# Performance work log

Hardware: AMD Instinct MI355X
Metric: run time of the kernel (lower is better)

Reference implementation:

```python
import jax, jax.numpy as jnp
import numpy as np

N = 50000
E = 800000
EPS = 1e-5


def graph_conv(x, src, dst, ew, W_rel, b_rel, W_root):
    # PyG GraphConv (aggr='add'): lin_rel(sum_j e_ij * x_j) + lin_root(x_i)
    msg = x[src] * ew[:, None]                      # [E, F_in]
    agg = jax.ops.segment_sum(msg, dst, num_segments=N)  # [N, F_in]
    return agg @ W_rel.T + b_rel + x @ W_root.T


def batchnorm_relu(h, gamma, beta):
    mu = jnp.mean(h, axis=0)
    var = jnp.mean(jnp.square(h - mu), axis=0)
    hn = (h - mu) * jax.lax.rsqrt(var + EPS)
    return jax.nn.relu(hn * gamma + beta)


def setup_inputs() -> dict:
    key = jax.random.key(0)
    ks = jax.random.split(key, 16)
    d_in, h, d_out = 128, 256, 64

    def lin(k, fo, fi):
        return jax.random.normal(k, (fo, fi), jnp.float32) * (1.0 / np.sqrt(fi))

    return {
        "x": jax.random.normal(ks[0], (N, d_in), jnp.float32),
        "edge_index": jax.random.randint(ks[1], (2, E), 0, N, jnp.int32),
        "edge_weight": jax.random.uniform(ks[2], (E,), jnp.float32),
        "Wr0": lin(ks[3], h, d_in), "br0": jnp.zeros((h,), jnp.float32), "Wt0": lin(ks[4], h, d_in),
        "g0": jnp.ones((h,), jnp.float32), "be0": jnp.zeros((h,), jnp.float32),
        "Wr1": lin(ks[5], h, h), "br1": jnp.zeros((h,), jnp.float32), "Wt1": lin(ks[6], h, h),
        "g1": jnp.ones((h,), jnp.float32), "be1": jnp.zeros((h,), jnp.float32),
        "Wr2": lin(ks[7], d_out, h), "br2": jnp.zeros((d_out,), jnp.float32), "Wt2": lin(ks[8], d_out, h),
    }


def reference(x, edge_index, edge_weight, Wr0, br0, Wt0, g0, be0,
              Wr1, br1, Wt1, g1, be1, Wr2, br2, Wt2):
    src, dst = edge_index[0], edge_index[1]
    h = graph_conv(x, src, dst, edge_weight, Wr0, br0, Wt0)
    h = batchnorm_relu(h, g0, be0)
    h = graph_conv(h, src, dst, edge_weight, Wr1, br1, Wt1)
    h = batchnorm_relu(h, g1, be1)
    return graph_conv(h, src, dst, edge_weight, Wr2, br2, Wt2)
```

## Files before the change

### kernel.cpp

```cpp
#include <hip/hip_runtime.h>
#include <cstddef>
#include <cstdint>

#define SCAN_B 512

using bf16x8 = __attribute__((ext_vector_type(8))) short;
using f32x4  = __attribute__((ext_vector_type(4))) float;

__device__ __forceinline__ unsigned short f2bf(float f) {
    unsigned int u = __builtin_bit_cast(unsigned int, f);
    return (unsigned short)((u + 0x7FFFu + ((u >> 16) & 1u)) >> 16);
}
__device__ __forceinline__ float bf2f(unsigned short b) {
    unsigned int u = ((unsigned int)b) << 16;
    return __builtin_bit_cast(float, u);
}
__device__ __forceinline__ float i2f(int i) { return __builtin_bit_cast(float, i); }
__device__ __forceinline__ void gload_lds16(const void* g, void* l) {
    __builtin_amdgcn_global_load_lds((const __attribute__((address_space(1))) void*)g,
                                     (__attribute__((address_space(3))) void*)l, 16, 0, 0);
}

__global__ void hist_rank_k(const int* __restrict__ dst, int* __restrict__ counts,
                            int* __restrict__ rank, int E) {
    int e = blockIdx.x * blockDim.x + threadIdx.x;
    if (e >= E) return;
    rank[e] = atomicAdd(&counts[dst[e]], 1);
}

__global__ void scan1_k(const int* __restrict__ counts, int* __restrict__ partial,
                        int* __restrict__ blocksum, int Nn) {
    __shared__ int sh[SCAN_B];
    int i = blockIdx.x * SCAN_B + threadIdx.x;
    int v = (i < Nn) ? counts[i] : 0;
    sh[threadIdx.x] = v;
    __syncthreads();
    for (int off = 1; off < SCAN_B; off <<= 1) {
        int t = (threadIdx.x >= (unsigned)off) ? sh[threadIdx.x - off] : 0;
        __syncthreads();
        sh[threadIdx.x] += t;
        __syncthreads();
    }
    if (i < Nn) partial[i] = sh[threadIdx.x];
    if (threadIdx.x == SCAN_B - 1) blocksum[blockIdx.x] = sh[threadIdx.x];
}

__global__ void scan2_k(int* __restrict__ blocksum, int nb) {
    __shared__ int sh[256];
    int v = (threadIdx.x < (unsigned)nb) ? blocksum[threadIdx.x] : 0;
    sh[threadIdx.x] = v;
    __syncthreads();
    for (int off = 1; off < 256; off <<= 1) {
        int t = (threadIdx.x >= (unsigned)off) ? sh[threadIdx.x - off] : 0;
        __syncthreads();
        sh[threadIdx.x] += t;
        __syncthreads();
    }
    if (threadIdx.x < (unsigned)nb) blocksum[threadIdx.x] = sh[threadIdx.x];
}

__global__ void scan3_k(const int* __restrict__ partial, const int* __restrict__ blocksum,
                        int* __restrict__ offsets, int Nn) {
    int i = blockIdx.x * SCAN_B + threadIdx.x;
    if (i >= Nn) return;
    int add = (blockIdx.x > 0) ? blocksum[blockIdx.x - 1] : 0;
    offsets[i + 1] = partial[i] + add;
    if (i == 0) offsets[0] = 0;
}

__global__ void fill2_k(const int* __restrict__ src, const int* __restrict__ dst,
                        const float* __restrict__ ew, const int* __restrict__ offsets,
                        const int* __restrict__ rank, int2* __restrict__ e_sw, int E) {
    int e = blockIdx.x * blockDim.x + threadIdx.x;
    if (e >= E) return;
    int d = dst[e];
    int pos = offsets[d] + rank[e];
    e_sw[pos] = make_int2(src[e], __builtin_bit_cast(int, ew[e]));
}

__global__ void f2bf_all_k(const float* __restrict__ x, const float* __restrict__ Wr0,
                           const float* __restrict__ Wt0, const float* __restrict__ Wr1,
                           const float* __restrict__ Wt1, const float* __restrict__ Wr2,
                           const float* __restrict__ Wt2, unsigned short* __restrict__ x_bf,
                           unsigned short* __restrict__ Wr0b, unsigned short* __restrict__ Wt0b,
                           unsigned short* __restrict__ Wr1b, unsigned short* __restrict__ Wt1b,
                           unsigned short* __restrict__ Wr2b, unsigned short* __restrict__ Wt2b,
                           int n4x) {
    int j = blockIdx.x * blockDim.x + threadIdx.x;
    const float* s;
    unsigned short* d;
    if (j < n4x) { s = x; d = x_bf; }
    else {
        j -= n4x;
        if (j < 8192) { s = Wr0; d = Wr0b; }
        else { j -= 8192;
        if (j < 8192) { s = Wt0; d = Wt0b; }
        else { j -= 8192;
        if (j < 16384) { s = Wr1; d = Wr1b; }
        else { j -= 16384;
        if (j < 16384) { s = Wt1; d = Wt1b; }
        else { j -= 16384;
        if (j < 4096) { s = Wr2; d = Wr2b; }
        else { j -= 4096;
        if (j >= 4096) return;
        s = Wt2; d = Wt2b; } } } } }
    }
    float4 v = reinterpret_cast<const float4*>(s)[j];
    ushort4 o;
    o.x = f2bf(v.x); o.y = f2bf(v.y); o.z = f2bf(v.z); o.w = f2bf(v.w);
    reinterpret_cast<ushort4*>(d)[j] = o;
}

template<int F>
__global__ void gather_bf_k(const unsigned short* __restrict__ x, const int* __restrict__ offsets,
                            const int2* __restrict__ e_sw, unsigned short* __restrict__ agg, int Nn) {
    int wid = (blockIdx.x * blockDim.x + threadIdx.x) >> 6;
    int lane = threadIdx.x & 63;
    if (wid >= Nn) return;
    int p = offsets[wid], end = offsets[wid + 1];
    if constexpr (F == 256) {
        float a0 = 0.f, a1 = 0.f, a2 = 0.f, a3 = 0.f;
        for (; p + 8 <= end; p += 8) {
            int2 ee[8];
            #pragma unroll
            for (int i = 0; i < 8; ++i) ee[i] = e_sw[p + i];
            ushort4 vv[8];
            #pragma unroll
            for (int i = 0; i < 8; ++i)
                vv[i] = *reinterpret_cast<const ushort4*>(x + (size_t)ee[i].x * F + lane * 4);
            #pragma unroll
            for (int i = 0; i < 8; ++i) {
                float w = i2f(ee[i].y);
                a0 += w * bf2f(vv[i].x); a1 += w * bf2f(vv[i].y);
                a2 += w * bf2f(vv[i].z); a3 += w * bf2f(vv[i].w);
            }
        }
        for (; p + 4 <= end; p += 4) {
            int2 ee[4];
            #pragma unroll
            for (int i = 0; i < 4; ++i) ee[i] = e_sw[p + i];
            ushort4 vv[4];
            #pragma unroll
            for (int i = 0; i < 4; ++i)
                vv[i] = *reinterpret_cast<const ushort4*>(x + (size_t)ee[i].x * F + lane * 4);
            #pragma unroll
            for (int i = 0; i < 4; ++i) {
                float w = i2f(ee[i].y);
                a0 += w * bf2f(vv[i].x); a1 += w * bf2f(vv[i].y);
                a2 += w * bf2f(vv[i].z); a3 += w * bf2f(vv[i].w);
            }
        }
        for (; p < end; ++p) {
            int2 e0 = e_sw[p];
            ushort4 v0 = *reinterpret_cast<const ushort4*>(x + (size_t)e0.x * F + lane * 4);
            float w0 = i2f(e0.y);
            a0 += w0 * bf2f(v0.x); a1 += w0 * bf2f(v0.y);
            a2 += w0 * bf2f(v0.z); a3 += w0 * bf2f(v0.w);
        }
        ushort4 o;
        o.x = f2bf(a0); o.y = f2bf(a1); o.z = f2bf(a2); o.w = f2bf(a3);
        *reinterpret_cast<ushort4*>(agg + (size_t)wid * F + lane * 4) = o;
    } else {
        float a0 = 0.f, a1 = 0.f;
        for (; p + 8 <= end; p += 8) {
            int2 ee[8];
            #pragma unroll
            for (int i = 0; i < 8; ++i) ee[i] = e_sw[p + i];
            unsigned int vv[8];
            #pragma unroll
            for (int i = 0; i < 8; ++i)
                vv[i] = *reinterpret_cast<const unsigned int*>(x + (size_t)ee[i].x * F + lane * 2);
            #pragma unroll
            for (int i = 0; i < 8; ++i) {
                float w = i2f(ee[i].y);
                a0 += w * bf2f((unsigned short)vv[i]);
                a1 += w * bf2f((unsigned short)(vv[i] >> 16));
            }
        }
        for (; p < end; ++p) {
            int2 e0 = e_sw[p];
            unsigned int v0 = *reinterpret_cast<const unsigned int*>(x + (size_t)e0.x * F + lane * 2);
            float w0 = i2f(e0.y);
            a0 += w0 * bf2f((unsigned short)v0);
            a1 += w0 * bf2f((unsigned short)(v0 >> 16));
        }
        unsigned int o = (unsigned int)f2bf(a0) | ((unsigned int)f2bf(a1) << 16);
        *reinterpret_cast<unsigned int*>(agg + (size_t)wid * F + lane * 2) = o;
    }
}

__global__ void gather_out_k(const unsigned short* __restrict__ t, const float* __restrict__ root,
                             const int* __restrict__ offsets, const int2* __restrict__ e_sw,
                             float* __restrict__ out, int Nn) {
    int gt = blockIdx.x * blockDim.x + threadIdx.x;
    int node = gt >> 4;
    int li = gt & 15;
    if (node >= Nn) return;
    int p = offsets[node], end = offsets[node + 1];
    float a0 = 0.f, a1 = 0.f, a2 = 0.f, a3 = 0.f;
    for (; p + 8 <= end; p += 8) {
        int2 ee[8];
        #pragma unroll
        for (int i = 0; i < 8; ++i) ee[i] = e_sw[p + i];
        ushort4 vv[8];
        #pragma unroll
        for (int i = 0; i < 8; ++i)
            vv[i] = *reinterpret_cast<const ushort4*>(t + (size_t)ee[i].x * 64 + li * 4);
        #pragma unroll
        for (int i = 0; i < 8; ++i) {
            float w = i2f(ee[i].y);
            a0 += w * bf2f(vv[i].x); a1 += w * bf2f(vv[i].y);
            a2 += w * bf2f(vv[i].z); a3 += w * bf2f(vv[i].w);
        }
    }
    for (; p < end; ++p) {
        int2 e0 = e_sw[p];
        ushort4 v0 = *reinterpret_cast<const ushort4*>(t + (size_t)e0.x * 64 + li * 4);
        float w0 = i2f(e0.y);
        a0 += w0 * bf2f(v0.x); a1 += w0 * bf2f(v0.y);
        a2 += w0 * bf2f(v0.z); a3 += w0 * bf2f(v0.w);
    }
    float4 r = *reinterpret_cast<const float4*>(root + (size_t)node * 64 + li * 4);
    float4 o = make_float4(r.x + a0, r.y + a1, r.z + a2, r.w + a3);
    *reinterpret_cast<float4*>(out + (size_t)node * 64 + li * 4) = o;
}

template<int K, int O, int BM, int BN, int MODE>
__global__ __launch_bounds__(256) void gemm_mfma_k(
        const unsigned short* __restrict__ A, const unsigned short* __restrict__ Wa,
        const unsigned short* __restrict__ X, const unsigned short* __restrict__ Wb,
        const float* __restrict__ bias, unsigned short* __restrict__ out_bf,
        float* __restrict__ out_f, float* __restrict__ sums, float* __restrict__ sumsq,
        int Nn) {
    constexpr int MI = BM / 16;
    constexpr int OJ = BN / 64;
    constexpr int KSTEPS = K / 64;
    constexpr int NT = (MODE == 0 ? 2 : 1) * KSTEPS;
    constexpr int ACH = BM / 32;
    constexpr int BCH = BN / 32;
    __shared__ unsigned short As[2][BM * 64];
    __shared__ unsigned short Bs[2][BN * 64];
    const int tid = threadIdx.x;
    const int w = tid >> 6, l = tid & 63;
    const int lrow = l & 15, kgrp = l >> 4;
    int bx = blockIdx.x;
    bx = (bx & 7) * (gridDim.x >> 3) + (bx >> 3);
    const int m0 = bx * BM;
    const int n0 = blockIdx.y * BN;

    auto stage = [&](int buf, int t) {
        int ph = t / KSTEPS;
        int k0 = (t % KSTEPS) * 64;
        const unsigned short* Ap = (MODE == 0 && ph) ? X : A;
        const unsigned short* Wp = (MODE == 0 && ph) ? Wb : Wa;
        #pragma unroll
        for (int i = 0; i < ACH; ++i) {
            int c = i * 256 + tid;
            int row = c >> 3, slot = c & 7;
            gload_lds16(Ap + (size_t)(m0 + row) * K + k0 + ((slot ^ (row & 7)) << 3),
                        &As[buf][(i * 256 + w * 64) * 8]);
        }
        #pragma unroll
        for (int i = 0; i < BCH; ++i) {
            int c = i * 256 + tid;
            int row = c >> 3, slot = c & 7;
            gload_lds16(Wp + (size_t)(n0 + row) * K + k0 + ((slot ^ (row & 7)) << 3),
                        &Bs[buf][(i * 256 + w * 64) * 8]);
        }
    };

    f32x4 acc[MI][OJ];
    #pragma unroll
    for (int i = 0; i < MI; ++i)
        #pragma unroll
        for (int j = 0; j < OJ; ++j) {
            f32x4 z = {0.f, 0.f, 0.f, 0.f};
            acc[i][j] = z;
        }

    stage(0, 0);
    __syncthreads();
    #pragma unroll
    for (int t = 0; t < NT; ++t) {
        const int cur = t & 1;
        if (t + 1 < NT) stage(cur ^ 1, t + 1);
        #pragma unroll
        for (int ks = 0; ks < 2; ++ks) {
            bf16x8 a[MI], b[OJ];
            #pragma unroll
            for (int mi = 0; mi < MI; ++mi) {
                int row = mi * 16 + lrow;
                int slot = (ks * 4 + kgrp) ^ (row & 7);
                a[mi] = *reinterpret_cast<const bf16x8*>(&As[cur][row * 64 + slot * 8]);
            }
            #pragma unroll
            for (int oj = 0; oj < OJ; ++oj) {
                int row = w * (OJ * 16) + oj * 16 + lrow;
                int slot = (ks * 4 + kgrp) ^ (row & 7);
                b[oj] = *reinterpret_cast<const bf16x8*>(&Bs[cur][row * 64 + slot * 8]);
            }
            #pragma unroll
            for (int mi = 0; mi < MI; ++mi)
                #pragma unroll
                for (int oj = 0; oj < OJ; ++oj)
                    acc[mi][oj] = __builtin_amdgcn_mfma_f32_16x16x32_bf16(
                        a[mi], b[oj], acc[mi][oj], 0, 0, 0);
        }
        __syncthreads();
    }

    if constexpr (MODE == 0) {
        #pragma unroll
        for (int oj = 0; oj < OJ; ++oj) {
            int col = n0 + w * (OJ * 16) + oj * 16 + lrow;
            float bcol = bias[col];
            float s = 0.f, q = 0.f;
            #pragma unroll
            for (int mi = 0; mi < MI; ++mi) {
                #pragma unroll
                for (int r = 0; r < 4; ++r) {
                    int row = m0 + mi * 16 + kgrp * 4 + r;
                    float v = acc[mi][oj][r] + bcol;
                    if (row < Nn) {
                        out_bf[(size_t)row * O + col] = f2bf(v);
                        s += v; q += v * v;
                    }
                }
            }
            s += __shfl_xor(s, 16, 64); q += __shfl_xor(q, 16, 64);
            s += __shfl_xor(s, 32, 64); q += __shfl_xor(q, 32, 64);
            if (kgrp == 0) {
                atomicAdd(&sums[col], s);
                atomicAdd(&sumsq[col], q);
            }
        }
    } else {
        #pragma unroll
        for (int oj = 0; oj < OJ; ++oj) {
            int col = n0 + w * (OJ * 16) + oj * 16 + lrow;
            #pragma unroll
            for (int mi = 0; mi < MI; ++mi) {
                #pragma unroll
                for (int r = 0; r < 4; ++r) {
                    int row = m0 + mi * 16 + kgrp * 4 + r;
                    if (row < Nn) {
                        if (col < 64)
                            out_bf[(size_t)row * 64 + col] = f2bf(acc[mi][oj][r]);
                        else
                            out_f[(size_t)row * 64 + (col - 64)] = acc[mi][oj][r] + bias[col - 64];
                    }
                }
            }
        }
    }
}

__global__ void bn_coef_k(const float* __restrict__ sums, const float* __restrict__ sumsq,
                          const float* __restrict__ g, const float* __restrict__ be,
                          float* __restrict__ scale, float* __restrict__ shift, float invN) {
    int f = threadIdx.x;
    float mu = sums[f] * invN;
    float var = sumsq[f] * invN - mu * mu;
    float sc = g[f] * rsqrtf(var + 1e-5f);
    scale[f] = sc;
    shift[f] = be[f] - mu * sc;
}

__global__ void bn_relu_bf_k(const unsigned short* __restrict__ h, const float* __restrict__ scale,
                             const float* __restrict__ shift, unsigned short* __restrict__ hb,
                             int total4) {
    int t = blockIdx.x * blockDim.x + threadIdx.x;
    if (t >= total4) return;
    int f0 = (t & 63) * 4;
    ushort4 v = reinterpret_cast<const ushort4*>(h)[t];
    float4 sc = *reinterpret_cast<const float4*>(scale + f0);
    float4 sh = *reinterpret_cast<const float4*>(shift + f0);
    ushort4 o;
    o.x = f2bf(fmaxf(bf2f(v.x) * sc.x + sh.x, 0.f));
    o.y = f2bf(fmaxf(bf2f(v.y) * sc.y + sh.y, 0.f));
    o.z = f2bf(fmaxf(bf2f(v.z) * sc.z + sh.z, 0.f));
    o.w = f2bf(fmaxf(bf2f(v.w) * sc.w + sh.w, 0.f));
    reinterpret_cast<ushort4*>(hb)[t] = o;
}

extern "C" void kernel_launch(void* const* d_in, const int* in_sizes, int n_in,
                              void* d_out, int out_size, void* d_ws, size_t ws_size,
                              hipStream_t stream) {
    const float* x   = (const float*)d_in[0];
    const int*   ei  = (const int*)d_in[1];
    const float* ew  = (const float*)d_in[2];
    const float* Wr0 = (const float*)d_in[3];
    const float* br0 = (const float*)d_in[4];
    const float* Wt0 = (const float*)d_in[5];
    const float* g0  = (const float*)d_in[6];
    const float* be0 = (const float*)d_in[7];
    const float* Wr1 = (const float*)d_in[8];
    const float* br1 = (const float*)d_in[9];
    const float* Wt1 = (const float*)d_in[10];
    const float* g1  = (const float*)d_in[11];
    const float* be1 = (const float*)d_in[12];
    const float* Wr2 = (const float*)d_in[13];
    const float* br2 = (const float*)d_in[14];
    const float* Wt2 = (const float*)d_in[15];

    const int E  = in_sizes[2];
    const int Nn = in_sizes[0] / 128;
    const size_t NP = 50176;
    const int* src = ei;
    const int* dst = ei + E;

    unsigned short* x_bf   = (unsigned short*)d_ws;
    unsigned short* agg_bf = x_bf + NP * 128;
    unsigned short* h0N    = agg_bf + NP * 256;
    unsigned short* h1N    = h0N + NP * 256;
    unsigned short* h_bf   = h1N + NP * 256;
    unsigned short* t_bf   = h_bf + NP * 256;
    unsigned short* wbf    = t_bf + NP * 64;
    unsigned short* Wr0b = wbf;
    unsigned short* Wt0b = wbf + 32768;
    unsigned short* Wr1b = wbf + 65536;
    unsigned short* Wt1b = wbf + 131072;
    unsigned short* W2cat = wbf + 196608;
    float* root  = (float*)(wbf + 229376);
    int2*  e_sw  = (int2*)(root + NP * 64);
    float* stats = (float*)(e_sw + E);
    int*   counts  = (int*)(stats + 4096);
    int*   partial = counts + Nn;
    int*   blocksum = partial + Nn;
    int*   rank    = blocksum + 512;
    int*   offsets = rank + E;

    dim3 blk(256);
    const int nbScan = (Nn + SCAN_B - 1) / SCAN_B;
    const float invN = 1.0f / (float)Nn;
    const int n4x = Nn * 32;

    hipMemsetAsync(stats, 0, (4096 + (size_t)Nn) * sizeof(float), stream);

    hist_rank_k<<<dim3((E + 255) / 256), blk, 0, stream>>>(dst, counts, rank, E);
    scan1_k<<<dim3(nbScan), dim3(SCAN_B), 0, stream>>>(counts, partial, blocksum, Nn);
    scan2_k<<<dim3(1), dim3(256), 0, stream>>>(blocksum, nbScan);
    scan3_k<<<dim3(nbScan), dim3(SCAN_B), 0, stream>>>(partial, blocksum, offsets, Nn);
    fill2_k<<<dim3((E + 255) / 256), blk, 0, stream>>>(src, dst, ew, offsets, rank, e_sw, E);

    f2bf_all_k<<<dim3((n4x + 57344 + 255) / 256), blk, 0, stream>>>(
        x, Wr0, Wt0, Wr1, Wt1, Wr2, Wt2,
        x_bf, Wr0b, Wt0b, Wr1b, Wt1b, W2cat, W2cat + 16384, n4x);

    const int gatherBlocks = (Nn * 64 + 255) / 256;

    gather_bf_k<128><<<dim3(gatherBlocks), blk, 0, stream>>>(x_bf, offsets, e_sw, agg_bf, Nn);
    gemm_mfma_k<128, 256, 128, 128, 0><<<dim3(NP / 128, 2), blk, 0, stream>>>(
        agg_bf, Wr0b, x_bf, Wt0b, br0, h_bf, nullptr, stats + 0, stats + 256, Nn);
    bn_coef_k<<<dim3(1), blk, 0, stream>>>(stats + 0, stats + 256, g0, be0,
                                           stats + 512, stats + 768, invN);
    bn_relu_bf_k<<<dim3((Nn * 64 + 255) / 256), blk, 0, stream>>>(
        h_bf, stats + 512, stats + 768, h0N, Nn * 64);

    gather_bf_k<256><<<dim3(gatherBlocks), blk, 0, stream>>>(h0N, offsets, e_sw, agg_bf, Nn);
    gemm_mfma_k<256, 256, 128, 128, 0><<<dim3(NP / 128, 2), blk, 0, stream>>>(
        agg_bf, Wr1b, h0N, Wt1b, br1, h_bf, nullptr, stats + 1024, stats + 1280, Nn);
    bn_coef_k<<<dim3(1), blk, 0, stream>>>(stats + 1024, stats + 1280, g1, be1,
                                           stats + 1536, stats + 1792, invN);
    bn_relu_bf_k<<<dim3((Nn * 64 + 255) / 256), blk, 0, stream>>>(
        h_bf, stats + 1536, stats + 1792, h1N, Nn * 64);

    gemm_mfma_k<256, 128, 128, 128, 1><<<dim3(NP / 128, 1), blk, 0, stream>>>(
        h1N, W2cat, nullptr, nullptr, br2, t_bf, root, nullptr, nullptr, Nn);
    gather_out_k<<<dim3((Nn * 16 + 255) / 256), blk, 0, stream>>>(
        t_bf, root, offsets, e_sw, (float*)d_out, Nn);
}
```

Before: 313.9 us.

## Fuse histogram with conversion, fold BN coefs, widen GEMM blocks, tidy gather addressing

The edge histogram and the fp32-to-bf16 conversion now run as one kernel, and the BN coefficient kernel is folded into bn_relu, which removes several launches. The GEMM moves to 512-thread blocks with a 2x4 wave grid, so each wave holds fewer accumulator tiles. The gather kernels use 32-bit byte-offset addressing, a scalar wave id and bit-mask bf16 unpacking, and the 4-edge unrolled tail loop is dropped. The trade-offs are that per-element BN recomputes rsqrt in every thread, and the GEMM register and occupancy behaviour changes.

```diff
diff --git a/kernel.cpp b/kernel.cpp
--- a/kernel.cpp
+++ b/kernel.cpp
@@ -16,77 +16,28 @@
     return __builtin_bit_cast(float, u);
 }
 __device__ __forceinline__ float i2f(int i) { return __builtin_bit_cast(float, i); }
+__device__ __forceinline__ float u2f(unsigned int u) { return __builtin_bit_cast(float, u); }
 __device__ __forceinline__ void gload_lds16(const void* g, void* l) {
     __builtin_amdgcn_global_load_lds((const __attribute__((address_space(1))) void*)g,
                                      (__attribute__((address_space(3))) void*)l, 16, 0, 0);
 }
 
-__global__ void hist_rank_k(const int* __restrict__ dst, int* __restrict__ counts,
-                            int* __restrict__ rank, int E) {
-    int e = blockIdx.x * blockDim.x + threadIdx.x;
-    if (e >= E) return;
-    rank[e] = atomicAdd(&counts[dst[e]], 1);
-}
-
-__global__ void scan1_k(const int* __restrict__ counts, int* __restrict__ partial,
-                        int* __restrict__ blocksum, int Nn) {
-    __shared__ int sh[SCAN_B];
-    int i = blockIdx.x * SCAN_B + threadIdx.x;
-    int v = (i < Nn) ? counts[i] : 0;
-    sh[threadIdx.x] = v;
-    __syncthreads();
-    for (int off = 1; off < SCAN_B; off <<= 1) {
-        int t = (threadIdx.x >= (unsigned)off) ? sh[threadIdx.x - off] : 0;
-        __syncthreads();
-        sh[threadIdx.x] += t;
-        __syncthreads();
-    }
-    if (i < Nn) partial[i] = sh[threadIdx.x];
-    if (threadIdx.x == SCAN_B - 1) blocksum[blockIdx.x] = sh[threadIdx.x];
-}
-
-__global__ void scan2_k(int* __restrict__ blocksum, int nb) {
-    __shared__ int sh[256];
-    int v = (threadIdx.x < (unsigned)nb) ? blocksum[threadIdx.x] : 0;
-    sh[threadIdx.x] = v;
-    __syncthreads();
-    for (int off = 1; off < 256; off <<= 1) {
-        int t = (threadIdx.x >= (unsigned)off) ? sh[threadIdx.x - off] : 0;
-        __syncthreads();
-        sh[threadIdx.x] += t;
-        __syncthreads();
-    }
-    if (threadIdx.x < (unsigned)nb) blocksum[threadIdx.x] = sh[threadIdx.x];
-}
-
-__global__ void scan3_k(const int* __restrict__ partial, const int* __restrict__ blocksum,
-                        int* __restrict__ offsets, int Nn) {
-    int i = blockIdx.x * SCAN_B + threadIdx.x;
-    if (i >= Nn) return;
-    int add = (blockIdx.x > 0) ? blocksum[blockIdx.x - 1] : 0;
-    offsets[i + 1] = partial[i] + add;
-    if (i == 0) offsets[0] = 0;
-}
-
-__global__ void fill2_k(const int* __restrict__ src, const int* __restrict__ dst,
-                        const float* __restrict__ ew, const int* __restrict__ offsets,
-                        const int* __restrict__ rank, int2* __restrict__ e_sw, int E) {
-    int e = blockIdx.x * blockDim.x + threadIdx.x;
-    if (e >= E) return;
-    int d = dst[e];
-    int pos = offsets[d] + rank[e];
-    e_sw[pos] = make_int2(src[e], __builtin_bit_cast(int, ew[e]));
-}
-
-__global__ void f2bf_all_k(const float* __restrict__ x, const float* __restrict__ Wr0,
-                           const float* __restrict__ Wt0, const float* __restrict__ Wr1,
-                           const float* __restrict__ Wt1, const float* __restrict__ Wr2,
-                           const float* __restrict__ Wt2, unsigned short* __restrict__ x_bf,
-                           unsigned short* __restrict__ Wr0b, unsigned short* __restrict__ Wt0b,
-                           unsigned short* __restrict__ Wr1b, unsigned short* __restrict__ Wt1b,
-                           unsigned short* __restrict__ Wr2b, unsigned short* __restrict__ Wt2b,
-                           int n4x) {
-    int j = blockIdx.x * blockDim.x + threadIdx.x;
+__global__ void hist_conv_k(const int* __restrict__ dst, int* __restrict__ counts,
+                            int* __restrict__ rank, int E, int histBlocks,
+                            const float* __restrict__ x, const float* __restrict__ Wr0,
+                            const float* __restrict__ Wt0, const float* __restrict__ Wr1,
+                            const float* __restrict__ Wt1, const float* __restrict__ Wr2,
+                            const float* __restrict__ Wt2, unsigned short* __restrict__ x_bf,
+                            unsigned short* __restrict__ Wr0b, unsigned short* __restrict__ Wt0b,
+                            unsigned short* __restrict__ Wr1b, unsigned short* __restrict__ Wt1b,
+                            unsigned short* __restrict__ Wr2b, unsigned short* __restrict__ Wt2b,
+                            int n4x) {
+    if ((int)blockIdx.x < histBlocks) {
+        int e = blockIdx.x * 256 + threadIdx.x;
+        if (e < E) rank[e] = atomicAdd(&counts[dst[e]], 1);
+        return;
+    }
+    int j = (blockIdx.x - histBlocks) * 256 + threadIdx.x;
     const float* s;
     unsigned short* d;
     if (j < n4x) { s = x; d = x_bf; }
@@ -111,81 +62,118 @@
     reinterpret_cast<ushort4*>(d)[j] = o;
 }
 
+__global__ void scan1_k(const int* __restrict__ counts, int* __restrict__ partial,
+                        int* __restrict__ blocksum, int Nn) {
+    __shared__ int sh[SCAN_B];
+    int i = blockIdx.x * SCAN_B + threadIdx.x;
+    int v = (i < Nn) ? counts[i] : 0;
+    sh[threadIdx.x] = v;
+    __syncthreads();
+    for (int off = 1; off < SCAN_B; off <<= 1) {
+        int t = (threadIdx.x >= (unsigned)off) ? sh[threadIdx.x - off] : 0;
+        __syncthreads();
+        sh[threadIdx.x] += t;
+        __syncthreads();
+    }
+    if (i < Nn) partial[i] = sh[threadIdx.x];
+    if (threadIdx.x == SCAN_B - 1) blocksum[blockIdx.x] = sh[threadIdx.x];
+}
+
+__global__ void scan2_k(int* __restrict__ blocksum, int nb) {
+    __shared__ int sh[256];
+    int v = (threadIdx.x < (unsigned)nb) ? blocksum[threadIdx.x] : 0;
+    sh[threadIdx.x] = v;
+    __syncthreads();
+    for (int off = 1; off < 256; off <<= 1) {
+        int t = (threadIdx.x >= (unsigned)off) ? sh[threadIdx.x - off] : 0;
+        __syncthreads();
+        sh[threadIdx.x] += t;
+        __syncthreads();
+    }
+    if (threadIdx.x < (unsigned)nb) blocksum[threadIdx.x] = sh[threadIdx.x];
+}
+
+__global__ void scan3_k(const int* __restrict__ partial, const int* __restrict__ blocksum,
+                        int* __restrict__ offsets, int Nn) {
+    int i = blockIdx.x * SCAN_B + threadIdx.x;
+    if (i >= Nn) return;
+    int add = (blockIdx.x > 0) ? blocksum[blockIdx.x - 1] : 0;
+    offsets[i + 1] = partial[i] + add;
+    if (i == 0) offsets[0] = 0;
+}
+
+__global__ void fill2_k(const int* __restrict__ src, const int* __restrict__ dst,
+                        const float* __restrict__ ew, const int* __restrict__ offsets,
+                        const int* __restrict__ rank, int2* __restrict__ e_sw, int E) {
+    int e = blockIdx.x * blockDim.x + threadIdx.x;
+    if (e >= E) return;
+    int d = dst[e];
+    int pos = offsets[d] + rank[e];
+    e_sw[pos] = make_int2(src[e], __builtin_bit_cast(int, ew[e]));
+}
+
 template<int F>
 __global__ void gather_bf_k(const unsigned short* __restrict__ x, const int* __restrict__ offsets,
                             const int2* __restrict__ e_sw, unsigned short* __restrict__ agg, int Nn) {
-    int wid = (blockIdx.x * blockDim.x + threadIdx.x) >> 6;
+    int wid = __builtin_amdgcn_readfirstlane((blockIdx.x * blockDim.x + threadIdx.x) >> 6);
     int lane = threadIdx.x & 63;
     if (wid >= Nn) return;
     int p = offsets[wid], end = offsets[wid + 1];
+    const char* xb = (const char*)x;
     if constexpr (F == 256) {
+        const unsigned loff = lane * 8u;
         float a0 = 0.f, a1 = 0.f, a2 = 0.f, a3 = 0.f;
         for (; p + 8 <= end; p += 8) {
             int2 ee[8];
             #pragma unroll
             for (int i = 0; i < 8; ++i) ee[i] = e_sw[p + i];
-            ushort4 vv[8];
+            uint2 vv[8];
             #pragma unroll
             for (int i = 0; i < 8; ++i)
-                vv[i] = *reinterpret_cast<const ushort4*>(x + (size_t)ee[i].x * F + lane * 4);
+                vv[i] = *reinterpret_cast<const uint2*>(xb + ((unsigned)ee[i].x * 512u + loff));
             #pragma unroll
             for (int i = 0; i < 8; ++i) {
                 float w = i2f(ee[i].y);
-                a0 += w * bf2f(vv[i].x); a1 += w * bf2f(vv[i].y);
-                a2 += w * bf2f(vv[i].z); a3 += w * bf2f(vv[i].w);
-            }
-        }
-        for (; p + 4 <= end; p += 4) {
-            int2 ee[4];
-            #pragma unroll
-            for (int i = 0; i < 4; ++i) ee[i] = e_sw[p + i];
-            ushort4 vv[4];
-            #pragma unroll
-            for (int i = 0; i < 4; ++i)
-                vv[i] = *reinterpret_cast<const ushort4*>(x + (size_t)ee[i].x * F + lane * 4);
-            #pragma unroll
-            for (int i = 0; i < 4; ++i) {
-                float w = i2f(ee[i].y);
-                a0 += w * bf2f(vv[i].x); a1 += w * bf2f(vv[i].y);
-                a2 += w * bf2f(vv[i].z); a3 += w * bf2f(vv[i].w);
+                a0 += w * u2f(vv[i].x << 16); a1 += w * u2f(vv[i].x & 0xFFFF0000u);
+                a2 += w * u2f(vv[i].y << 16); a3 += w * u2f(vv[i].y & 0xFFFF0000u);
             }
         }
         for (; p < end; ++p) {
             int2 e0 = e_sw[p];
-            ushort4 v0 = *reinterpret_cast<const ushort4*>(x + (size_t)e0.x * F + lane * 4);
-            float w0 = i2f(e0.y);
-            a0 += w0 * bf2f(v0.x); a1 += w0 * bf2f(v0.y);
-            a2 += w0 * bf2f(v0.z); a3 += w0 * bf2f(v0.w);
-        }
-        ushort4 o;
-        o.x = f2bf(a0); o.y = f2bf(a1); o.z = f2bf(a2); o.w = f2bf(a3);
-        *reinterpret_cast<ushort4*>(agg + (size_t)wid * F + lane * 4) = o;
+            uint2 v0 = *reinterpret_cast<const uint2*>(xb + ((unsigned)e0.x * 512u + loff));
+            float w = i2f(e0.y);
+            a0 += w * u2f(v0.x << 16); a1 += w * u2f(v0.x & 0xFFFF0000u);
+            a2 += w * u2f(v0.y << 16); a3 += w * u2f(v0.y & 0xFFFF0000u);
+        }
+        uint2 o;
+        o.x = (unsigned)f2bf(a0) | ((unsigned)f2bf(a1) << 16);
+        o.y = (unsigned)f2bf(a2) | ((unsigned)f2bf(a3) << 16);
+        *reinterpret_cast<uint2*>(agg + (size_t)wid * 256 + lane * 4) = o;
     } else {
+        const unsigned loff = lane * 4u;
         float a0 = 0.f, a1 = 0.f;
         for (; p + 8 <= end; p += 8) {
             int2 ee[8];
             #pragma unroll
             for (int i = 0; i < 8; ++i) ee[i] = e_sw[p + i];
-            unsigned int vv[8];
+            unsigned vv[8];
             #pragma unroll
             for (int i = 0; i < 8; ++i)
-                vv[i] = *reinterpret_cast<const unsigned int*>(x + (size_t)ee[i].x * F + lane * 2);
+                vv[i] = *reinterpret_cast<const unsigned*>(xb + ((unsigned)ee[i].x * 256u + loff));
             #pragma unroll
             for (int i = 0; i < 8; ++i) {
                 float w = i2f(ee[i].y);
-                a0 += w * bf2f((unsigned short)vv[i]);
-                a1 += w * bf2f((unsigned short)(vv[i] >> 16));
+                a0 += w * u2f(vv[i] << 16); a1 += w * u2f(vv[i] & 0xFFFF0000u);
             }
         }
         for (; p < end; ++p) {
             int2 e0 = e_sw[p];
-            unsigned int v0 = *reinterpret_cast<const unsigned int*>(x + (size_t)e0.x * F + lane * 2);
-            float w0 = i2f(e0.y);
-            a0 += w0 * bf2f((unsigned short)v0);
-            a1 += w0 * bf2f((unsigned short)(v0 >> 16));
-        }
-        unsigned int o = (unsigned int)f2bf(a0) | ((unsigned int)f2bf(a1) << 16);
-        *reinterpret_cast<unsigned int*>(agg + (size_t)wid * F + lane * 2) = o;
+            unsigned v0 = *reinterpret_cast<const unsigned*>(xb + ((unsigned)e0.x * 256u + loff));
+            float w = i2f(e0.y);
+            a0 += w * u2f(v0 << 16); a1 += w * u2f(v0 & 0xFFFF0000u);
+        }
+        unsigned o = (unsigned)f2bf(a0) | ((unsigned)f2bf(a1) << 16);
+        *reinterpret_cast<unsigned*>(agg + (size_t)wid * 128 + lane * 2) = o;
     }
 }
 
@@ -197,28 +185,30 @@
     int li = gt & 15;
     if (node >= Nn) return;
     int p = offsets[node], end = offsets[node + 1];
+    const char* tb = (const char*)t;
+    const unsigned loff = li * 8u;
     float a0 = 0.f, a1 = 0.f, a2 = 0.f, a3 = 0.f;
     for (; p + 8 <= end; p += 8) {
         int2 ee[8];
         #pragma unroll
         for (int i = 0; i < 8; ++i) ee[i] = e_sw[p + i];
-        ushort4 vv[8];
+        uint2 vv[8];
         #pragma unroll
         for (int i = 0; i < 8; ++i)
-            vv[i] = *reinterpret_cast<const ushort4*>(t + (size_t)ee[i].x * 64 + li * 4);
+            vv[i] = *reinterpret_cast<const uint2*>(tb + ((unsigned)ee[i].x * 128u + loff));
         #pragma unroll
         for (int i = 0; i < 8; ++i) {
             float w = i2f(ee[i].y);
-            a0 += w * bf2f(vv[i].x); a1 += w * bf2f(vv[i].y);
-            a2 += w * bf2f(vv[i].z); a3 += w * bf2f(vv[i].w);
+            a0 += w * u2f(vv[i].x << 16); a1 += w * u2f(vv[i].x & 0xFFFF0000u);
+            a2 += w * u2f(vv[i].y << 16); a3 += w * u2f(vv[i].y & 0xFFFF0000u);
         }
     }
     for (; p < end; ++p) {
         int2 e0 = e_sw[p];
-        ushort4 v0 = *reinterpret_cast<const ushort4*>(t + (size_t)e0.x * 64 + li * 4);
-        float w0 = i2f(e0.y);
-        a0 += w0 * bf2f(v0.x); a1 += w0 * bf2f(v0.y);
-        a2 += w0 * bf2f(v0.z); a3 += w0 * bf2f(v0.w);
+        uint2 v0 = *reinterpret_cast<const uint2*>(tb + ((unsigned)e0.x * 128u + loff));
+        float w = i2f(e0.y);
+        a0 += w * u2f(v0.x << 16); a1 += w * u2f(v0.x & 0xFFFF0000u);
+        a2 += w * u2f(v0.y << 16); a3 += w * u2f(v0.y & 0xFFFF0000u);
     }
     float4 r = *reinterpret_cast<const float4*>(root + (size_t)node * 64 + li * 4);
     float4 o = make_float4(r.x + a0, r.y + a1, r.z + a2, r.w + a3);
@@ -226,22 +216,23 @@
 }
 
 template<int K, int O, int BM, int BN, int MODE>
-__global__ __launch_bounds__(256) void gemm_mfma_k(
+__global__ __launch_bounds__(512, 4) void gemm_mfma_k(
         const unsigned short* __restrict__ A, const unsigned short* __restrict__ Wa,
         const unsigned short* __restrict__ X, const unsigned short* __restrict__ Wb,
         const float* __restrict__ bias, unsigned short* __restrict__ out_bf,
         float* __restrict__ out_f, float* __restrict__ sums, float* __restrict__ sumsq,
         int Nn) {
-    constexpr int MI = BM / 16;
+    constexpr int MI = BM / 32;
     constexpr int OJ = BN / 64;
     constexpr int KSTEPS = K / 64;
     constexpr int NT = (MODE == 0 ? 2 : 1) * KSTEPS;
-    constexpr int ACH = BM / 32;
-    constexpr int BCH = BN / 32;
+    constexpr int ACH = BM / 64;
+    constexpr int BCH = BN / 64;
     __shared__ unsigned short As[2][BM * 64];
     __shared__ unsigned short Bs[2][BN * 64];
     const int tid = threadIdx.x;
     const int w = tid >> 6, l = tid & 63;
+    const int wr = w >> 2, wc = w & 3;
     const int lrow = l & 15, kgrp = l >> 4;
     int bx = blockIdx.x;
     bx = (bx & 7) * (gridDim.x >> 3) + (bx >> 3);
@@ -255,17 +246,17 @@
         const unsigned short* Wp = (MODE == 0 && ph) ? Wb : Wa;
         #pragma unroll
         for (int i = 0; i < ACH; ++i) {
-            int c = i * 256 + tid;
+            int c = i * 512 + tid;
             int row = c >> 3, slot = c & 7;
             gload_lds16(Ap + (size_t)(m0 + row) * K + k0 + ((slot ^ (row & 7)) << 3),
-                        &As[buf][(i * 256 + w * 64) * 8]);
+                        &As[buf][(i * 512 + w * 64) * 8]);
         }
         #pragma unroll
         for (int i = 0; i < BCH; ++i) {
-            int c = i * 256 + tid;
+            int c = i * 512 + tid;
             int row = c >> 3, slot = c & 7;
             gload_lds16(Wp + (size_t)(n0 + row) * K + k0 + ((slot ^ (row & 7)) << 3),
-                        &Bs[buf][(i * 256 + w * 64) * 8]);
+                        &Bs[buf][(i * 512 + w * 64) * 8]);
         }
     };
 
@@ -289,13 +280,13 @@
             bf16x8 a[MI], b[OJ];
             #pragma unroll
             for (int mi = 0; mi < MI; ++mi) {
-                int row = mi * 16 + lrow;
+                int row = wr * 64 + mi * 16 + lrow;
                 int slot = (ks * 4 + kgrp) ^ (row & 7);
                 a[mi] = *reinterpret_cast<const bf16x8*>(&As[cur][row * 64 + slot * 8]);
             }
             #pragma unroll
             for (int oj = 0; oj < OJ; ++oj) {
-                int row = w * (OJ * 16) + oj * 16 + lrow;
+                int row = wc * 32 + oj * 16 + lrow;
                 int slot = (ks * 4 + kgrp) ^ (row & 7);
                 b[oj] = *reinterpret_cast<const bf16x8*>(&Bs[cur][row * 64 + slot * 8]);
             }
@@ -312,14 +303,14 @@
     if constexpr (MODE == 0) {
         #pragma unroll
         for (int oj = 0; oj < OJ; ++oj) {
-            int col = n0 + w * (OJ * 16) + oj * 16 + lrow;
+            int col = n0 + wc * 32 + oj * 16 + lrow;
             float bcol = bias[col];
             float s = 0.f, q = 0.f;
             #pragma unroll
             for (int mi = 0; mi < MI; ++mi) {
                 #pragma unroll
                 for (int r = 0; r < 4; ++r) {
-                    int row = m0 + mi * 16 + kgrp * 4 + r;
+                    int row = m0 + wr * 64 + mi * 16 + kgrp * 4 + r;
                     float v = acc[mi][oj][r] + bcol;
                     if (row < Nn) {
                         out_bf[(size_t)row * O + col] = f2bf(v);
@@ -337,12 +328,12 @@
     } else {
         #pragma unroll
         for (int oj = 0; oj < OJ; ++oj) {
-            int col = n0 + w * (OJ * 16) + oj * 16 + lrow;
+            int col = n0 + wc * 32 + oj * 16 + lrow;
             #pragma unroll
             for (int mi = 0; mi < MI; ++mi) {
                 #pragma unroll
                 for (int r = 0; r < 4; ++r) {
-                    int row = m0 + mi * 16 + kgrp * 4 + r;
+                    int row = m0 + wr * 64 + mi * 16 + kgrp * 4 + r;
                     if (row < Nn) {
                         if (col < 64)
                             out_bf[(size_t)row * 64 + col] = f2bf(acc[mi][oj][r]);
@@ -355,31 +346,33 @@
     }
 }
 
-__global__ void bn_coef_k(const float* __restrict__ sums, const float* __restrict__ sumsq,
-                          const float* __restrict__ g, const float* __restrict__ be,
-                          float* __restrict__ scale, float* __restrict__ shift, float invN) {
-    int f = threadIdx.x;
-    float mu = sums[f] * invN;
-    float var = sumsq[f] * invN - mu * mu;
-    float sc = g[f] * rsqrtf(var + 1e-5f);
-    scale[f] = sc;
-    shift[f] = be[f] - mu * sc;
-}
-
-__global__ void bn_relu_bf_k(const unsigned short* __restrict__ h, const float* __restrict__ scale,
-                             const float* __restrict__ shift, unsigned short* __restrict__ hb,
-                             int total4) {
+__global__ void bn_relu_bf_k(const unsigned short* __restrict__ h, const float* __restrict__ sums,
+                             const float* __restrict__ sumsq, const float* __restrict__ g,
+                             const float* __restrict__ be, unsigned short* __restrict__ hb,
+                             float invN, int total4) {
     int t = blockIdx.x * blockDim.x + threadIdx.x;
     if (t >= total4) return;
     int f0 = (t & 63) * 4;
+    float4 sm = *reinterpret_cast<const float4*>(sums + f0);
+    float4 sq = *reinterpret_cast<const float4*>(sumsq + f0);
+    float4 gg = *reinterpret_cast<const float4*>(g + f0);
+    float4 bb = *reinterpret_cast<const float4*>(be + f0);
+    float smv[4] = {sm.x, sm.y, sm.z, sm.w};
+    float sqv[4] = {sq.x, sq.y, sq.z, sq.w};
+    float ggv[4] = {gg.x, gg.y, gg.z, gg.w};
+    float bbv[4] = {bb.x, bb.y, bb.z, bb.w};
     ushort4 v = reinterpret_cast<const ushort4*>(h)[t];
-    float4 sc = *reinterpret_cast<const float4*>(scale + f0);
-    float4 sh = *reinterpret_cast<const float4*>(shift + f0);
+    unsigned short vv[4] = {v.x, v.y, v.z, v.w};
     ushort4 o;
-    o.x = f2bf(fmaxf(bf2f(v.x) * sc.x + sh.x, 0.f));
-    o.y = f2bf(fmaxf(bf2f(v.y) * sc.y + sh.y, 0.f));
-    o.z = f2bf(fmaxf(bf2f(v.z) * sc.z + sh.z, 0.f));
-    o.w = f2bf(fmaxf(bf2f(v.w) * sc.w + sh.w, 0.f));
+    unsigned short* op = &o.x;
+    #pragma unroll
+    for (int c = 0; c < 4; ++c) {
+        float mu = smv[c] * invN;
+        float var = sqv[c] * invN - mu * mu;
+        float sc = ggv[c] * rsqrtf(var + 1e-5f);
+        float sh = bbv[c] - mu * sc;
+        op[c] = f2bf(fmaxf(bf2f(vv[c]) * sc + sh, 0.f));
+    }
     reinterpret_cast<ushort4*>(hb)[t] = o;
 }
 
@@ -434,38 +427,35 @@
     const int nbScan = (Nn + SCAN_B - 1) / SCAN_B;
     const float invN = 1.0f / (float)Nn;
     const int n4x = Nn * 32;
+    const int histBlocks = (E + 255) / 256;
+    const int convBlocks = (n4x + 57344 + 255) / 256;
 
     hipMemsetAsync(stats, 0, (4096 + (size_t)Nn) * sizeof(float), stream);
 
-    hist_rank_k<<<dim3((E + 255) / 256), blk, 0, stream>>>(dst, counts, rank, E);
+    hist_conv_k<<<dim3(histBlocks + convBlocks), blk, 0, stream>>>(
+        dst, counts, rank, E, histBlocks,
+        x, Wr0, Wt0, Wr1, Wt1, Wr2, Wt2,
+        x_bf, Wr0b, Wt0b, Wr1b, Wt1b, W2cat, W2cat + 16384, n4x);
     scan1_k<<<dim3(nbScan), dim3(SCAN_B), 0, stream>>>(counts, partial, blocksum, Nn);
     scan2_k<<<dim3(1), dim3(256), 0, stream>>>(blocksum, nbScan);
     scan3_k<<<dim3(nbScan), dim3(SCAN_B), 0, stream>>>(partial, blocksum, offsets, Nn);
-    fill2_k<<<dim3((E + 255) / 256), blk, 0, stream>>>(src, dst, ew, offsets, rank, e_sw, E);
-
-    f2bf_all_k<<<dim3((n4x + 57344 + 255) / 256), blk, 0, stream>>>(
-        x, Wr0, Wt0, Wr1, Wt1, Wr2, Wt2,
-        x_bf, Wr0b, Wt0b, Wr1b, Wt1b, W2cat, W2cat + 16384, n4x);
+    fill2_k<<<dim3(histBlocks), blk, 0, stream>>>(src, dst, ew, offsets, rank, e_sw, E);
 
     const int gatherBlocks = (Nn * 64 + 255) / 256;
 
     gather_bf_k<128><<<dim3(gatherBlocks), blk, 0, stream>>>(x_bf, offsets, e_sw, agg_bf, Nn);
-    gemm_mfma_k<128, 256, 128, 128, 0><<<dim3(NP / 128, 2), blk, 0, stream>>>(
+    gemm_mfma_k<128, 256, 128, 128, 0><<<dim3(NP / 128, 2), dim3(512), 0, stream>>>(
         agg_bf, Wr0b, x_bf, Wt0b, br0, h_bf, nullptr, stats + 0, stats + 256, Nn);
-    bn_coef_k<<<dim3(1), blk, 0, stream>>>(stats + 0, stats + 256, g0, be0,
-                                           stats + 512, stats + 768, invN);
     bn_relu_bf_k<<<dim3((Nn * 64 + 255) / 256), blk, 0, stream>>>(
-        h_bf, stats + 512, stats + 768, h0N, Nn * 64);
+        h_bf, stats + 0, stats + 256, g0, be0, h0N, invN, Nn * 64);
 
     gather_bf_k<256><<<dim3(gatherBlocks), blk, 0, stream>>>(h0N, offsets, e_sw, agg_bf, Nn);
-    gemm_mfma_k<256, 256, 128, 128, 0><<<dim3(NP / 128, 2), blk, 0, stream>>>(
+    gemm_mfma_k<256, 256, 128, 128, 0><<<dim3(NP / 128, 2), dim3(512), 0, stream>>>(
         agg_bf, Wr1b, h0N, Wt1b, br1, h_bf, nullptr, stats + 1024, stats + 1280, Nn);
-    bn_coef_k<<<dim3(1), blk, 0, stream>>>(stats + 1024, stats + 1280, g1, be1,
-                                           stats + 1536, stats + 1792, invN);
     bn_relu_bf_k<<<dim3((Nn * 64 + 255) / 256), blk, 0, stream>>>(
-        h_bf, stats + 1536, stats + 1792, h1N, Nn * 64);
-
-    gemm_mfma_k<256, 128, 128, 128, 1><<<dim3(NP / 128, 1), blk, 0, stream>>>(
+        h_bf, stats + 1024, stats + 1280, g1, be1, h1N, invN, Nn * 64);
+
+    gemm_mfma_k<256, 128, 128, 128, 1><<<dim3(NP / 128, 1), dim3(512), 0, stream>>>(
         h1N, W2cat, nullptr, nullptr, br2, t_bf, root, nullptr, nullptr, Nn);
     gather_out_k<<<dim3((Nn * 16 + 255) / 256), blk, 0, stream>>>(
         t_bf, root, offsets, e_sw, (float*)d_out, Nn);
```

Result: faster. 304.6 us (-2.9%).
